# Kernel optimization log

Measured on AMD Instinct MI355X. Metric: run time of the kernel, lower is better.

Reference implementation:

```python
import jax, jax.numpy as jnp
import numpy as np
from jax.scipy.special import erf

# synthetic covalent radii table (original imports `covalent_radii`, e.g. from ase)
COV_RADII = jnp.asarray(0.3 + 0.02 * np.arange(100), dtype=jnp.float32)

B_MOL = 1024   # molecules per batch
N_ATOM = 128   # atoms per molecule (equal-sized ragged batch, atoms sorted by molecule)
N_ELEM = 10


def setup_inputs() -> dict:
    key = jax.random.key(0)
    ks = jax.random.split(key, 6)
    N = B_MOL * N_ATOM
    return {
        "eneg": jax.random.normal(ks[0], (N, 1), jnp.float32),
        "positions": jax.random.normal(ks[1], (N, 3), jnp.float32) * 3.0,
        "node_attrs": jax.random.uniform(ks[2], (N, N_ELEM), jnp.float32),
        "hardness": jax.random.uniform(ks[3], (N_ELEM,), jnp.float32),
        "total_charge": jax.random.normal(ks[4], (B_MOL,), jnp.float32),
        "batch": jnp.repeat(jnp.arange(B_MOL), N_ATOM),          # sorted molecule ids
        "atomic_numbers": jax.random.randint(ks[5], (N,), 1, 90),
    }


def reference(eneg, positions, node_attrs, hardness, total_charge, batch, atomic_numbers):
    # atoms are sorted by molecule with equal molecule sizes, so the ragged
    # python loop of the original collapses to a batched [B, n, ...] computation.
    B = total_charge.shape[0]
    N = positions.shape[0]
    n = N // B
    sqrt_pi = jnp.sqrt(jnp.asarray(np.pi, jnp.float32))
    sqrt_2 = jnp.sqrt(jnp.asarray(2.0, jnp.float32))

    pos = positions.reshape(B, n, 3)
    Z = atomic_numbers.reshape(B, n)
    atom_idx = jnp.argmax(node_attrs, axis=1).reshape(B, n)

    r = COV_RADII[Z]                                     # [B, n]
    diag_vals = hardness[atom_idx] + 1.0 / (sqrt_pi * r)  # [B, n]
    sigma = jnp.square(r)                                # [B, n]
    gamma = jnp.sqrt(sigma[:, :, None] + sigma[:, None, :])  # [B, n, n]

    diff = pos[:, :, None, :] - pos[:, None, :, :]       # [B, n, n, 3]
    sq = jnp.sum(diff * diff, axis=-1)                   # [B, n, n]
    eye = jnp.eye(n, dtype=bool)
    dist = jnp.sqrt(jnp.where(eye, 1.0, sq))             # safe diag (overwritten below)

    A = erf(dist / (sqrt_2 * gamma)) / dist              # [B, n, n]
    A = jnp.where(eye, diag_vals[:, :, None], A)         # scatter hardness diagonal

    # augment with charge-conservation row/column of ones (corner = 1)
    A = jnp.concatenate([A, jnp.ones((B, n, 1), A.dtype)], axis=2)
    A = jnp.concatenate([A, jnp.ones((B, 1, n + 1), A.dtype)], axis=1)

    b = jnp.concatenate([-eneg.reshape(B, n, 1),
                         total_charge.reshape(B, 1, 1)], axis=1)  # [B, n+1, 1]

    x = jnp.linalg.solve(A, b)                           # batched small solves
    return x[:, :n, 0].reshape(-1)                       # partial charges, [N]
```

## Files before the change

kernel.cpp:

```cpp
#include <hip/hip_runtime.h>
#include <math.h>

#define NMOL  1024
#define N     128
#define NELEM 10
#define BLOCK 256
#define PW    8
#define NPAN  16
#define PSTR  12
#define USTR  132

typedef __attribute__((ext_vector_type(4))) float f4;


__global__ __launch_bounds__(BLOCK, 2) void ceq_solve_kernel(
    const float* __restrict__ eneg,
    const float* __restrict__ positions,
    const float* __restrict__ node_attrs,
    const float* __restrict__ hardness,
    const float* __restrict__ total_charge,
    const int*   __restrict__ atomic_numbers,
    float* __restrict__ out)
{
    __shared__ __align__(16) float P[2][N * PSTR];
    __shared__ __align__(16) float Up[2][PW * USTR];
    __shared__ __align__(16) float Ublk[2][NPAN][PW][PW];
    __shared__ float Dinv[2][PW], Dd[2][PW];
    __shared__ float rhsY[2][N], rhsZ[2][N];
    __shared__ float sxY[2][N], sxZ[2][N];
    __shared__ float px[2][N], py[2][N], pz[2][N], sg[2][N], dgv[2][N];
    __shared__ float lamS[2];

    const int tid  = threadIdx.x;
    const int lane = tid & 63;
    const int g    = tid >> 7;
    const int gt   = tid & 127;
    const int wv   = (tid >> 6) & 1;
    const int r0   = 2 * lane;
    const int r1   = r0 + 1;
    const int mol  = 2 * blockIdx.x + g;
    const int base = mol * N;

    {
        const int i = gt;
        const int Z = atomic_numbers[base + i];
        const float rad = 0.3f + 0.02f * (float)Z;
        sg[g][i] = rad * rad;
        const float* na = node_attrs + (size_t)(base + i) * NELEM;
        float best = na[0]; int bi = 0;
        #pragma unroll
        for (int e = 1; e < NELEM; ++e) {
            float v = na[e];
            if (v > best) { best = v; bi = e; }
        }
        dgv[g][i] = hardness[bi] + 0.5641895835477563f / rad;
        const float* p = positions + (size_t)(base + i) * 3;
        px[g][i] = p[0]; py[g][i] = p[1]; pz[g][i] = p[2];
        rhsY[g][i] = -eneg[base + i];
        rhsZ[g][i] = 1.0f;
    }
    __syncthreads();

    f4 Ar0[16], Ar1[16];
    {
        const float x0 = px[g][r0], y0 = py[g][r0], z0 = pz[g][r0];
        const float s0 = sg[g][r0], d0 = dgv[g][r0];
        const float x1 = px[g][r1], y1 = py[g][r1], z1 = pz[g][r1];
        const float s1 = sg[g][r1], d1 = dgv[g][r1];
        #pragma unroll
        for (int c = 0; c < 16; ++c) {
            const int jb = 16 * (c >> 1) + 8 * wv + 4 * (c & 1);
            f4 v0, v1;
            #pragma unroll
            for (int e = 0; e < 4; ++e) {
                const int j = jb + e;
                float a0, a1;
                if (j == r0) a0 = d0;
                else {
                    const float dx = x0 - px[g][j], dy = y0 - py[g][j], dz = z0 - pz[g][j];
                    const float d = sqrtf(dx * dx + dy * dy + dz * dz);
                    a0 = erff(d / (1.4142135623730951f * sqrtf(s0 + sg[g][j]))) / d;
                }
                if (j == r1) a1 = d1;
                else {
                    const float dx = x1 - px[g][j], dy = y1 - py[g][j], dz = z1 - pz[g][j];
                    const float d = sqrtf(dx * dx + dy * dy + dz * dz);
                    a1 = erff(d / (1.4142135623730951f * sqrtf(s1 + sg[g][j]))) / d;
                }
                ((float*)&v0)[e] = a0;
                ((float*)&v1)[e] = a1;
            }
            Ar0[c] = v0;
            Ar1[c] = v1;
        }
    }

    for (int p = 0; p < NPAN; ++p) {
        const int k0 = PW * p;
        const int q  = (p >> 1) & 7;

        if (wv == (p & 1) && lane >= 4 * p) {
            f4 a00, a01, a10, a11;
            switch (q) {
                case 0:  a00 = Ar0[0];  a01 = Ar0[1];  a10 = Ar1[0];  a11 = Ar1[1];  break;
                case 1:  a00 = Ar0[2];  a01 = Ar0[3];  a10 = Ar1[2];  a11 = Ar1[3];  break;
                case 2:  a00 = Ar0[4];  a01 = Ar0[5];  a10 = Ar1[4];  a11 = Ar1[5];  break;
                case 3:  a00 = Ar0[6];  a01 = Ar0[7];  a10 = Ar1[6];  a11 = Ar1[7];  break;
                case 4:  a00 = Ar0[8];  a01 = Ar0[9];  a10 = Ar1[8];  a11 = Ar1[9];  break;
                case 5:  a00 = Ar0[10]; a01 = Ar0[11]; a10 = Ar1[10]; a11 = Ar1[11]; break;
                case 6:  a00 = Ar0[12]; a01 = Ar0[13]; a10 = Ar1[12]; a11 = Ar1[13]; break;
                default: a00 = Ar0[14]; a01 = Ar0[15]; a10 = Ar1[14]; a11 = Ar1[15]; break;
            }
            if (lane >= 4 * p + 4) {
                *(f4*)&P[g][r0 * PSTR + 0] = a00; *(f4*)&P[g][r0 * PSTR + 4] = a01;
                *(f4*)&P[g][r1 * PSTR + 0] = a10; *(f4*)&P[g][r1 * PSTR + 4] = a11;
            } else {
                float u0[PW] = { a00.x, a00.y, a00.z, a00.w, a01.x, a01.y, a01.z, a01.w };
                float u1[PW] = { a10.x, a10.y, a10.z, a10.w, a11.x, a11.y, a11.z, a11.w };
                float ry0 = rhsY[g][r0], rz0 = rhsZ[g][r0];
                float ry1 = rhsY[g][r1], rz1 = rhsZ[g][r1];
                const int rl = lane - 4 * p;
                #pragma unroll
                for (int kk = 0; kk < PW; ++kk) {
                    const int src = 4 * p + (kk >> 1);
                    float pr[PW];
                    #pragma unroll
                    for (int j = kk; j < PW; ++j)
                        pr[j] = __shfl((kk & 1) ? u1[j] : u0[j], src);
                    const float cY = __shfl((kk & 1) ? ry1 : ry0, src);
                    const float cZ = __shfl((kk & 1) ? rz1 : rz0, src);
                    const float dinv = 1.0f / pr[kk];
                    if (2 * rl > kk) {
                        const float m = u0[kk] * dinv; u0[kk] = m;
                        #pragma unroll
                        for (int j = kk + 1; j < PW; ++j) u0[j] -= m * pr[j];
                        ry0 -= m * cY; rz0 -= m * cZ;
                    }
                    if (2 * rl + 1 > kk) {
                        const float m = u1[kk] * dinv; u1[kk] = m;
                        #pragma unroll
                        for (int j = kk + 1; j < PW; ++j) u1[j] -= m * pr[j];
                        ry1 -= m * cY; rz1 -= m * cZ;
                    }
                    if (rl == (kk >> 1)) { Dinv[g][kk] = dinv; Dd[g][kk] = pr[kk]; }
                }
                f4 w0 = { u0[0], u0[1], u0[2], u0[3] }, w1 = { u0[4], u0[5], u0[6], u0[7] };
                *(f4*)&Ublk[g][p][2 * rl][0] = w0; *(f4*)&Ublk[g][p][2 * rl][4] = w1;
                f4 w2 = { u1[0], u1[1], u1[2], u1[3] }, w3 = { u1[4], u1[5], u1[6], u1[7] };
                *(f4*)&Ublk[g][p][2 * rl + 1][0] = w2; *(f4*)&Ublk[g][p][2 * rl + 1][4] = w3;
                rhsY[g][r0] = ry0; rhsZ[g][r0] = rz0;
                rhsY[g][r1] = ry1; rhsZ[g][r1] = rz1;
            }
        }
        __syncthreads();

        const int nb = (N - PW) - k0;
        if (gt < nb) {
            const int i = k0 + PW + gt;
            f4 a = *(const f4*)&P[g][i * PSTR], b = *(const f4*)&P[g][i * PSTR + 4];
            float av[PW] = { a.x, a.y, a.z, a.w, b.x, b.y, b.z, b.w };
            float m[PW];
            #pragma unroll
            for (int j = 0; j < PW; ++j) {
                float acc = av[j];
                #pragma unroll
                for (int t = 0; t < j; ++t) acc -= m[t] * Ublk[g][p][t][j];
                m[j] = acc * Dinv[g][j];
            }
            f4 ma = { m[0], m[1], m[2], m[3] }, mb = { m[4], m[5], m[6], m[7] };
            *(f4*)&P[g][i * PSTR]     = ma;
            *(f4*)&P[g][i * PSTR + 4] = mb;
            #pragma unroll
            for (int u = 0; u < PW; ++u) Up[g][u * USTR + i] = m[u] * Dd[g][u];
            float ry = rhsY[g][i], rz = rhsZ[g][i];
            #pragma unroll
            for (int t = 0; t < PW; ++t) {
                ry -= m[t] * rhsY[g][k0 + t];
                rz -= m[t] * rhsZ[g][k0 + t];
            }
            rhsY[g][i] = ry; rhsZ[g][i] = rz;
        }
        __syncthreads();

        if (lane >= 4 * p && lane < 4 * p + 4) {
            const int u0 = r0 - k0, u1 = u0 + 1;
            #pragma unroll
            for (int c = 0; c < 16; ++c) {
                const int t  = 2 * (c >> 1) + wv;
                const int gc = 4 * (c >> 1) + 2 * wv + (c & 1);
                if (t > p) {
                    Ar0[c] = *(const f4*)&Up[g][u0 * USTR + 4 * gc];
                    Ar1[c] = *(const f4*)&Up[g][u1 * USTR + 4 * gc];
                }
            }
        }
        const bool hasmat = (14 + wv) > p;
        if (hasmat && lane >= 4 * p + 4) {
            float lA0[PW], lA1[PW];
            {
                f4 a = *(const f4*)&P[g][r0 * PSTR], b = *(const f4*)&P[g][r0 * PSTR + 4];
                lA0[0]=a.x; lA0[1]=a.y; lA0[2]=a.z; lA0[3]=a.w;
                lA0[4]=b.x; lA0[5]=b.y; lA0[6]=b.z; lA0[7]=b.w;
                f4 c2 = *(const f4*)&P[g][r1 * PSTR], d2 = *(const f4*)&P[g][r1 * PSTR + 4];
                lA1[0]=c2.x; lA1[1]=c2.y; lA1[2]=c2.z; lA1[3]=c2.w;
                lA1[4]=d2.x; lA1[5]=d2.y; lA1[6]=d2.z; lA1[7]=d2.w;
            }
            #pragma unroll
            for (int c = 0; c < 16; ++c) {
                const int t  = 2 * (c >> 1) + wv;
                const int gc = 4 * (c >> 1) + 2 * wv + (c & 1);
                if (t > p) {
                    f4 acc0 = Ar0[c], acc1 = Ar1[c];
                    #pragma unroll
                    for (int u = 0; u < PW; ++u) {
                        const f4 uv = *(const f4*)&Up[g][u * USTR + 4 * gc];
                        acc0 -= uv * lA0[u];
                        acc1 -= uv * lA1[u];
                    }
                    Ar0[c] = acc0; Ar1[c] = acc1;
                }
            }
        }
        __syncthreads();
    }

    for (int pb = NPAN - 1; pb >= 0; --pb) {
        const int k0 = PW * pb;
        if (tid < 4) {
            const int gg = tid >> 1;
            float* rhs = (tid & 1) ? rhsZ[gg] : rhsY[gg];
            float* sx  = (tid & 1) ? sxZ[gg]  : sxY[gg];
            float x[PW];
            #pragma unroll
            for (int kk = PW - 1; kk >= 0; --kk) {
                float acc = rhs[k0 + kk];
                #pragma unroll
                for (int jj = kk + 1; jj < PW; ++jj) acc -= Ublk[gg][pb][kk][jj] * x[jj];
                x[kk] = acc / Ublk[gg][pb][kk][kk];
                sx[k0 + kk] = x[kk];
            }
        }
        __syncthreads();
        if (wv == (pb & 1) && lane < 4 * pb) {
            f4 a00, a01, a10, a11;
            switch ((pb >> 1) & 7) {
                case 0:  a00 = Ar0[0];  a01 = Ar0[1];  a10 = Ar1[0];  a11 = Ar1[1];  break;
                case 1:  a00 = Ar0[2];  a01 = Ar0[3];  a10 = Ar1[2];  a11 = Ar1[3];  break;
                case 2:  a00 = Ar0[4];  a01 = Ar0[5];  a10 = Ar1[4];  a11 = Ar1[5];  break;
                case 3:  a00 = Ar0[6];  a01 = Ar0[7];  a10 = Ar1[6];  a11 = Ar1[7];  break;
                case 4:  a00 = Ar0[8];  a01 = Ar0[9];  a10 = Ar1[8];  a11 = Ar1[9];  break;
                case 5:  a00 = Ar0[10]; a01 = Ar0[11]; a10 = Ar1[10]; a11 = Ar1[11]; break;
                case 6:  a00 = Ar0[12]; a01 = Ar0[13]; a10 = Ar1[12]; a11 = Ar1[13]; break;
                default: a00 = Ar0[14]; a01 = Ar0[15]; a10 = Ar1[14]; a11 = Ar1[15]; break;
            }
            float yy0 = rhsY[g][r0], yy1 = rhsY[g][r1];
            float zz0 = rhsZ[g][r0], zz1 = rhsZ[g][r1];
            yy0 -= a00.x*sxY[g][k0]   + a00.y*sxY[g][k0+1] + a00.z*sxY[g][k0+2] + a00.w*sxY[g][k0+3]
                 + a01.x*sxY[g][k0+4] + a01.y*sxY[g][k0+5] + a01.z*sxY[g][k0+6] + a01.w*sxY[g][k0+7];
            yy1 -= a10.x*sxY[g][k0]   + a10.y*sxY[g][k0+1] + a10.z*sxY[g][k0+2] + a10.w*sxY[g][k0+3]
                 + a11.x*sxY[g][k0+4] + a11.y*sxY[g][k0+5] + a11.z*sxY[g][k0+6] + a11.w*sxY[g][k0+7];
            zz0 -= a00.x*sxZ[g][k0]   + a00.y*sxZ[g][k0+1] + a00.z*sxZ[g][k0+2] + a00.w*sxZ[g][k0+3]
                 + a01.x*sxZ[g][k0+4] + a01.y*sxZ[g][k0+5] + a01.z*sxZ[g][k0+6] + a01.w*sxZ[g][k0+7];
            zz1 -= a10.x*sxZ[g][k0]   + a10.y*sxZ[g][k0+1] + a10.z*sxZ[g][k0+2] + a10.w*sxZ[g][k0+3]
                 + a11.x*sxZ[g][k0+4] + a11.y*sxZ[g][k0+5] + a11.z*sxZ[g][k0+6] + a11.w*sxZ[g][k0+7];
            rhsY[g][r0] = yy0; rhsY[g][r1] = yy1;
            rhsZ[g][r0] = zz0; rhsZ[g][r1] = zz1;
        }
        __syncthreads();
    }

    if (wv == 0) {
        float vY = sxY[g][lane] + sxY[g][lane + 64];
        float vZ = sxZ[g][lane] + sxZ[g][lane + 64];
        #pragma unroll
        for (int off = 32; off; off >>= 1) {
            vY += __shfl_xor(vY, off);
            vZ += __shfl_xor(vZ, off);
        }
        if (lane == 0) lamS[g] = (vY - total_charge[mol]) / (vZ - 1.0f);
    }
    __syncthreads();
    out[base + gt] = sxY[g][gt] - lamS[g] * sxZ[g][gt];
}

extern "C" void kernel_launch(void* const* d_in, const int* in_sizes, int n_in,
                              void* d_out, int out_size, void* d_ws, size_t ws_size,
                              hipStream_t stream) {
    const float* eneg           = (const float*)d_in[0];
    const float* positions      = (const float*)d_in[1];
    const float* node_attrs     = (const float*)d_in[2];
    const float* hardness       = (const float*)d_in[3];
    const float* total_charge   = (const float*)d_in[4];
    const int*   atomic_numbers = (const int*)d_in[6];
    float* out = (float*)d_out;

    ceq_solve_kernel<<<NMOL / 2, BLOCK, 0, stream>>>(
        eneg, positions, node_attrs, hardness, total_charge, atomic_numbers, out);
}
```

Measured before the change: 214.5 us.

## Widen LU panel width to 16 and alias staging arrays into panel buffer

Doubles the blocked LU panel width from 8 to 16, halving the number of panels and the barrier-separated factor/update phases. The register-resident matrix tile is remapped to a new column layout, and the back-substitution dot products are vectorised. Per-atom staging arrays now alias the panel shared buffer to offset the larger panel and Ublk storage, which needs an extra barrier. In exchange the serial in-panel factorization and triangular solves get longer, and register pressure rises.

Result: slower. 253.5 us (+18.2%).

```diff
diff --git a/kernel.cpp b/kernel.cpp
--- a/kernel.cpp
+++ b/kernel.cpp
@@ -5,9 +5,9 @@
 #define N     128
 #define NELEM 10
 #define BLOCK 256
-#define PW    8
-#define NPAN  16
-#define PSTR  12
+#define PW    16
+#define NPAN  8
+#define PSTR  20
 #define USTR  132
 
 typedef __attribute__((ext_vector_type(4))) float f4;
@@ -26,9 +26,8 @@
     __shared__ __align__(16) float Up[2][PW * USTR];
     __shared__ __align__(16) float Ublk[2][NPAN][PW][PW];
     __shared__ float Dinv[2][PW], Dd[2][PW];
-    __shared__ float rhsY[2][N], rhsZ[2][N];
-    __shared__ float sxY[2][N], sxZ[2][N];
-    __shared__ float px[2][N], py[2][N], pz[2][N], sg[2][N], dgv[2][N];
+    __shared__ __align__(16) float rhsY[2][N], rhsZ[2][N];
+    __shared__ __align__(16) float sxY[2][N], sxZ[2][N];
     __shared__ float lamS[2];
 
     const int tid  = threadIdx.x;
@@ -41,11 +40,17 @@
     const int mol  = 2 * blockIdx.x + g;
     const int base = mol * N;
 
+    float* px  = &P[g][0 * N];
+    float* py  = &P[g][1 * N];
+    float* pz  = &P[g][2 * N];
+    float* sg  = &P[g][3 * N];
+    float* dgv = &P[g][4 * N];
+
     {
         const int i = gt;
         const int Z = atomic_numbers[base + i];
         const float rad = 0.3f + 0.02f * (float)Z;
-        sg[g][i] = rad * rad;
+        sg[i] = rad * rad;
         const float* na = node_attrs + (size_t)(base + i) * NELEM;
         float best = na[0]; int bi = 0;
         #pragma unroll
@@ -53,9 +58,9 @@
             float v = na[e];
             if (v > best) { best = v; bi = e; }
         }
-        dgv[g][i] = hardness[bi] + 0.5641895835477563f / rad;
+        dgv[i] = hardness[bi] + 0.5641895835477563f / rad;
         const float* p = positions + (size_t)(base + i) * 3;
-        px[g][i] = p[0]; py[g][i] = p[1]; pz[g][i] = p[2];
+        px[i] = p[0]; py[i] = p[1]; pz[i] = p[2];
         rhsY[g][i] = -eneg[base + i];
         rhsZ[g][i] = 1.0f;
     }
@@ -63,13 +68,13 @@
 
     f4 Ar0[16], Ar1[16];
     {
-        const float x0 = px[g][r0], y0 = py[g][r0], z0 = pz[g][r0];
-        const float s0 = sg[g][r0], d0 = dgv[g][r0];
-        const float x1 = px[g][r1], y1 = py[g][r1], z1 = pz[g][r1];
-        const float s1 = sg[g][r1], d1 = dgv[g][r1];
+        const float x0 = px[r0], y0 = py[r0], z0 = pz[r0];
+        const float s0 = sg[r0], d0 = dgv[r0];
+        const float x1 = px[r1], y1 = py[r1], z1 = pz[r1];
+        const float s1 = sg[r1], d1 = dgv[r1];
         #pragma unroll
         for (int c = 0; c < 16; ++c) {
-            const int jb = 16 * (c >> 1) + 8 * wv + 4 * (c & 1);
+            const int jb = 32 * (c >> 2) + 16 * wv + 4 * (c & 3);
             f4 v0, v1;
             #pragma unroll
             for (int e = 0; e < 4; ++e) {
@@ -77,15 +82,15 @@
                 float a0, a1;
                 if (j == r0) a0 = d0;
                 else {
-                    const float dx = x0 - px[g][j], dy = y0 - py[g][j], dz = z0 - pz[g][j];
+                    const float dx = x0 - px[j], dy = y0 - py[j], dz = z0 - pz[j];
                     const float d = sqrtf(dx * dx + dy * dy + dz * dz);
-                    a0 = erff(d / (1.4142135623730951f * sqrtf(s0 + sg[g][j]))) / d;
+                    a0 = erff(d / (1.4142135623730951f * sqrtf(s0 + sg[j]))) / d;
                 }
                 if (j == r1) a1 = d1;
                 else {
-                    const float dx = x1 - px[g][j], dy = y1 - py[g][j], dz = z1 - pz[g][j];
+                    const float dx = x1 - px[j], dy = y1 - py[j], dz = z1 - pz[j];
                     const float d = sqrtf(dx * dx + dy * dy + dz * dz);
-                    a1 = erff(d / (1.4142135623730951f * sqrtf(s1 + sg[g][j]))) / d;
+                    a1 = erff(d / (1.4142135623730951f * sqrtf(s1 + sg[j]))) / d;
                 }
                 ((float*)&v0)[e] = a0;
                 ((float*)&v1)[e] = a1;
@@ -94,35 +99,40 @@
             Ar1[c] = v1;
         }
     }
+    __syncthreads();
 
     for (int p = 0; p < NPAN; ++p) {
         const int k0 = PW * p;
-        const int q  = (p >> 1) & 7;
-
-        if (wv == (p & 1) && lane >= 4 * p) {
-            f4 a00, a01, a10, a11;
-            switch (q) {
-                case 0:  a00 = Ar0[0];  a01 = Ar0[1];  a10 = Ar1[0];  a11 = Ar1[1];  break;
-                case 1:  a00 = Ar0[2];  a01 = Ar0[3];  a10 = Ar1[2];  a11 = Ar1[3];  break;
-                case 2:  a00 = Ar0[4];  a01 = Ar0[5];  a10 = Ar1[4];  a11 = Ar1[5];  break;
-                case 3:  a00 = Ar0[6];  a01 = Ar0[7];  a10 = Ar1[6];  a11 = Ar1[7];  break;
-                case 4:  a00 = Ar0[8];  a01 = Ar0[9];  a10 = Ar1[8];  a11 = Ar1[9];  break;
-                case 5:  a00 = Ar0[10]; a01 = Ar0[11]; a10 = Ar1[10]; a11 = Ar1[11]; break;
-                case 6:  a00 = Ar0[12]; a01 = Ar0[13]; a10 = Ar1[12]; a11 = Ar1[13]; break;
-                default: a00 = Ar0[14]; a01 = Ar0[15]; a10 = Ar1[14]; a11 = Ar1[15]; break;
-            }
-            if (lane >= 4 * p + 4) {
-                *(f4*)&P[g][r0 * PSTR + 0] = a00; *(f4*)&P[g][r0 * PSTR + 4] = a01;
-                *(f4*)&P[g][r1 * PSTR + 0] = a10; *(f4*)&P[g][r1 * PSTR + 4] = a11;
+        const int k  = p >> 1;
+
+        if (wv == (p & 1) && lane >= 8 * p) {
+            f4 a0, a1, a2, a3, b0, b1, b2, b3;
+            switch (k) {
+                case 0:  a0=Ar0[0];  a1=Ar0[1];  a2=Ar0[2];  a3=Ar0[3];
+                         b0=Ar1[0];  b1=Ar1[1];  b2=Ar1[2];  b3=Ar1[3];  break;
+                case 1:  a0=Ar0[4];  a1=Ar0[5];  a2=Ar0[6];  a3=Ar0[7];
+                         b0=Ar1[4];  b1=Ar1[5];  b2=Ar1[6];  b3=Ar1[7];  break;
+                case 2:  a0=Ar0[8];  a1=Ar0[9];  a2=Ar0[10]; a3=Ar0[11];
+                         b0=Ar1[8];  b1=Ar1[9];  b2=Ar1[10]; b3=Ar1[11]; break;
+                default: a0=Ar0[12]; a1=Ar0[13]; a2=Ar0[14]; a3=Ar0[15];
+                         b0=Ar1[12]; b1=Ar1[13]; b2=Ar1[14]; b3=Ar1[15]; break;
+            }
+            if (lane >= 8 * p + 8) {
+                *(f4*)&P[g][r0 * PSTR + 0] = a0; *(f4*)&P[g][r0 * PSTR + 4]  = a1;
+                *(f4*)&P[g][r0 * PSTR + 8] = a2; *(f4*)&P[g][r0 * PSTR + 12] = a3;
+                *(f4*)&P[g][r1 * PSTR + 0] = b0; *(f4*)&P[g][r1 * PSTR + 4]  = b1;
+                *(f4*)&P[g][r1 * PSTR + 8] = b2; *(f4*)&P[g][r1 * PSTR + 12] = b3;
             } else {
-                float u0[PW] = { a00.x, a00.y, a00.z, a00.w, a01.x, a01.y, a01.z, a01.w };
-                float u1[PW] = { a10.x, a10.y, a10.z, a10.w, a11.x, a11.y, a11.z, a11.w };
+                float u0[PW] = { a0.x,a0.y,a0.z,a0.w, a1.x,a1.y,a1.z,a1.w,
+                                 a2.x,a2.y,a2.z,a2.w, a3.x,a3.y,a3.z,a3.w };
+                float u1[PW] = { b0.x,b0.y,b0.z,b0.w, b1.x,b1.y,b1.z,b1.w,
+                                 b2.x,b2.y,b2.z,b2.w, b3.x,b3.y,b3.z,b3.w };
                 float ry0 = rhsY[g][r0], rz0 = rhsZ[g][r0];
                 float ry1 = rhsY[g][r1], rz1 = rhsZ[g][r1];
-                const int rl = lane - 4 * p;
+                const int rl = lane - 8 * p;
                 #pragma unroll
                 for (int kk = 0; kk < PW; ++kk) {
-                    const int src = 4 * p + (kk >> 1);
+                    const int src = 8 * p + (kk >> 1);
                     float pr[PW];
                     #pragma unroll
                     for (int j = kk; j < PW; ++j)
@@ -144,10 +154,15 @@
                     }
                     if (rl == (kk >> 1)) { Dinv[g][kk] = dinv; Dd[g][kk] = pr[kk]; }
                 }
-                f4 w0 = { u0[0], u0[1], u0[2], u0[3] }, w1 = { u0[4], u0[5], u0[6], u0[7] };
-                *(f4*)&Ublk[g][p][2 * rl][0] = w0; *(f4*)&Ublk[g][p][2 * rl][4] = w1;
-                f4 w2 = { u1[0], u1[1], u1[2], u1[3] }, w3 = { u1[4], u1[5], u1[6], u1[7] };
-                *(f4*)&Ublk[g][p][2 * rl + 1][0] = w2; *(f4*)&Ublk[g][p][2 * rl + 1][4] = w3;
+                f4 w;
+                w = (f4){u0[0],u0[1],u0[2],u0[3]};    *(f4*)&Ublk[g][p][2*rl][0]  = w;
+                w = (f4){u0[4],u0[5],u0[6],u0[7]};    *(f4*)&Ublk[g][p][2*rl][4]  = w;
+                w = (f4){u0[8],u0[9],u0[10],u0[11]};  *(f4*)&Ublk[g][p][2*rl][8]  = w;
+                w = (f4){u0[12],u0[13],u0[14],u0[15]};*(f4*)&Ublk[g][p][2*rl][12] = w;
+                w = (f4){u1[0],u1[1],u1[2],u1[3]};    *(f4*)&Ublk[g][p][2*rl+1][0]  = w;
+                w = (f4){u1[4],u1[5],u1[6],u1[7]};    *(f4*)&Ublk[g][p][2*rl+1][4]  = w;
+                w = (f4){u1[8],u1[9],u1[10],u1[11]};  *(f4*)&Ublk[g][p][2*rl+1][8]  = w;
+                w = (f4){u1[12],u1[13],u1[14],u1[15]};*(f4*)&Ublk[g][p][2*rl+1][12] = w;
                 rhsY[g][r0] = ry0; rhsZ[g][r0] = rz0;
                 rhsY[g][r1] = ry1; rhsZ[g][r1] = rz1;
             }
@@ -157,8 +172,10 @@
         const int nb = (N - PW) - k0;
         if (gt < nb) {
             const int i = k0 + PW + gt;
-            f4 a = *(const f4*)&P[g][i * PSTR], b = *(const f4*)&P[g][i * PSTR + 4];
-            float av[PW] = { a.x, a.y, a.z, a.w, b.x, b.y, b.z, b.w };
+            f4 A0 = *(const f4*)&P[g][i * PSTR + 0], A1 = *(const f4*)&P[g][i * PSTR + 4];
+            f4 A2 = *(const f4*)&P[g][i * PSTR + 8], A3 = *(const f4*)&P[g][i * PSTR + 12];
+            float av[PW] = { A0.x,A0.y,A0.z,A0.w, A1.x,A1.y,A1.z,A1.w,
+                             A2.x,A2.y,A2.z,A2.w, A3.x,A3.y,A3.z,A3.w };
             float m[PW];
             #pragma unroll
             for (int j = 0; j < PW; ++j) {
@@ -167,9 +184,11 @@
                 for (int t = 0; t < j; ++t) acc -= m[t] * Ublk[g][p][t][j];
                 m[j] = acc * Dinv[g][j];
             }
-            f4 ma = { m[0], m[1], m[2], m[3] }, mb = { m[4], m[5], m[6], m[7] };
-            *(f4*)&P[g][i * PSTR]     = ma;
-            *(f4*)&P[g][i * PSTR + 4] = mb;
+            f4 w;
+            w = (f4){m[0],m[1],m[2],m[3]};     *(f4*)&P[g][i * PSTR + 0]  = w;
+            w = (f4){m[4],m[5],m[6],m[7]};     *(f4*)&P[g][i * PSTR + 4]  = w;
+            w = (f4){m[8],m[9],m[10],m[11]};   *(f4*)&P[g][i * PSTR + 8]  = w;
+            w = (f4){m[12],m[13],m[14],m[15]}; *(f4*)&P[g][i * PSTR + 12] = w;
             #pragma unroll
             for (int u = 0; u < PW; ++u) Up[g][u * USTR + i] = m[u] * Dd[g][u];
             float ry = rhsY[g][i], rz = rhsZ[g][i];
@@ -182,38 +201,44 @@
         }
         __syncthreads();
 
-        if (lane >= 4 * p && lane < 4 * p + 4) {
-            const int u0 = r0 - k0, u1 = u0 + 1;
+        if (lane >= 8 * p && lane < 8 * p + 8) {
+            const int u0r = r0 - k0, u1r = u0r + 1;
             #pragma unroll
             for (int c = 0; c < 16; ++c) {
-                const int t  = 2 * (c >> 1) + wv;
-                const int gc = 4 * (c >> 1) + 2 * wv + (c & 1);
+                const int t  = 2 * (c >> 2) + wv;
+                const int jb = 32 * (c >> 2) + 16 * wv + 4 * (c & 3);
                 if (t > p) {
-                    Ar0[c] = *(const f4*)&Up[g][u0 * USTR + 4 * gc];
-                    Ar1[c] = *(const f4*)&Up[g][u1 * USTR + 4 * gc];
-                }
-            }
-        }
-        const bool hasmat = (14 + wv) > p;
-        if (hasmat && lane >= 4 * p + 4) {
+                    Ar0[c] = *(const f4*)&Up[g][u0r * USTR + jb];
+                    Ar1[c] = *(const f4*)&Up[g][u1r * USTR + jb];
+                }
+            }
+        }
+        const bool hasmat = (6 + wv) > p;
+        if (hasmat && lane >= 8 * p + 8) {
             float lA0[PW], lA1[PW];
             {
-                f4 a = *(const f4*)&P[g][r0 * PSTR], b = *(const f4*)&P[g][r0 * PSTR + 4];
+                f4 a = *(const f4*)&P[g][r0 * PSTR + 0], b = *(const f4*)&P[g][r0 * PSTR + 4];
+                f4 c2 = *(const f4*)&P[g][r0 * PSTR + 8], d2 = *(const f4*)&P[g][r0 * PSTR + 12];
                 lA0[0]=a.x; lA0[1]=a.y; lA0[2]=a.z; lA0[3]=a.w;
                 lA0[4]=b.x; lA0[5]=b.y; lA0[6]=b.z; lA0[7]=b.w;
-                f4 c2 = *(const f4*)&P[g][r1 * PSTR], d2 = *(const f4*)&P[g][r1 * PSTR + 4];
-                lA1[0]=c2.x; lA1[1]=c2.y; lA1[2]=c2.z; lA1[3]=c2.w;
-                lA1[4]=d2.x; lA1[5]=d2.y; lA1[6]=d2.z; lA1[7]=d2.w;
+                lA0[8]=c2.x; lA0[9]=c2.y; lA0[10]=c2.z; lA0[11]=c2.w;
+                lA0[12]=d2.x; lA0[13]=d2.y; lA0[14]=d2.z; lA0[15]=d2.w;
+                f4 e = *(const f4*)&P[g][r1 * PSTR + 0], f = *(const f4*)&P[g][r1 * PSTR + 4];
+                f4 h = *(const f4*)&P[g][r1 * PSTR + 8], i2 = *(const f4*)&P[g][r1 * PSTR + 12];
+                lA1[0]=e.x; lA1[1]=e.y; lA1[2]=e.z; lA1[3]=e.w;
+                lA1[4]=f.x; lA1[5]=f.y; lA1[6]=f.z; lA1[7]=f.w;
+                lA1[8]=h.x; lA1[9]=h.y; lA1[10]=h.z; lA1[11]=h.w;
+                lA1[12]=i2.x; lA1[13]=i2.y; lA1[14]=i2.z; lA1[15]=i2.w;
             }
             #pragma unroll
             for (int c = 0; c < 16; ++c) {
-                const int t  = 2 * (c >> 1) + wv;
-                const int gc = 4 * (c >> 1) + 2 * wv + (c & 1);
+                const int t  = 2 * (c >> 2) + wv;
+                const int jb = 32 * (c >> 2) + 16 * wv + 4 * (c & 3);
                 if (t > p) {
                     f4 acc0 = Ar0[c], acc1 = Ar1[c];
                     #pragma unroll
                     for (int u = 0; u < PW; ++u) {
-                        const f4 uv = *(const f4*)&Up[g][u * USTR + 4 * gc];
+                        const f4 uv = *(const f4*)&Up[g][u * USTR + jb];
                         acc0 -= uv * lA0[u];
                         acc1 -= uv * lA1[u];
                     }
@@ -241,30 +266,30 @@
             }
         }
         __syncthreads();
-        if (wv == (pb & 1) && lane < 4 * pb) {
-            f4 a00, a01, a10, a11;
-            switch ((pb >> 1) & 7) {
-                case 0:  a00 = Ar0[0];  a01 = Ar0[1];  a10 = Ar1[0];  a11 = Ar1[1];  break;
-                case 1:  a00 = Ar0[2];  a01 = Ar0[3];  a10 = Ar1[2];  a11 = Ar1[3];  break;
-                case 2:  a00 = Ar0[4];  a01 = Ar0[5];  a10 = Ar1[4];  a11 = Ar1[5];  break;
-                case 3:  a00 = Ar0[6];  a01 = Ar0[7];  a10 = Ar1[6];  a11 = Ar1[7];  break;
-                case 4:  a00 = Ar0[8];  a01 = Ar0[9];  a10 = Ar1[8];  a11 = Ar1[9];  break;
-                case 5:  a00 = Ar0[10]; a01 = Ar0[11]; a10 = Ar1[10]; a11 = Ar1[11]; break;
-                case 6:  a00 = Ar0[12]; a01 = Ar0[13]; a10 = Ar1[12]; a11 = Ar1[13]; break;
-                default: a00 = Ar0[14]; a01 = Ar0[15]; a10 = Ar1[14]; a11 = Ar1[15]; break;
-            }
-            float yy0 = rhsY[g][r0], yy1 = rhsY[g][r1];
-            float zz0 = rhsZ[g][r0], zz1 = rhsZ[g][r1];
-            yy0 -= a00.x*sxY[g][k0]   + a00.y*sxY[g][k0+1] + a00.z*sxY[g][k0+2] + a00.w*sxY[g][k0+3]
-                 + a01.x*sxY[g][k0+4] + a01.y*sxY[g][k0+5] + a01.z*sxY[g][k0+6] + a01.w*sxY[g][k0+7];
-            yy1 -= a10.x*sxY[g][k0]   + a10.y*sxY[g][k0+1] + a10.z*sxY[g][k0+2] + a10.w*sxY[g][k0+3]
-                 + a11.x*sxY[g][k0+4] + a11.y*sxY[g][k0+5] + a11.z*sxY[g][k0+6] + a11.w*sxY[g][k0+7];
-            zz0 -= a00.x*sxZ[g][k0]   + a00.y*sxZ[g][k0+1] + a00.z*sxZ[g][k0+2] + a00.w*sxZ[g][k0+3]
-                 + a01.x*sxZ[g][k0+4] + a01.y*sxZ[g][k0+5] + a01.z*sxZ[g][k0+6] + a01.w*sxZ[g][k0+7];
-            zz1 -= a10.x*sxZ[g][k0]   + a10.y*sxZ[g][k0+1] + a10.z*sxZ[g][k0+2] + a10.w*sxZ[g][k0+3]
-                 + a11.x*sxZ[g][k0+4] + a11.y*sxZ[g][k0+5] + a11.z*sxZ[g][k0+6] + a11.w*sxZ[g][k0+7];
-            rhsY[g][r0] = yy0; rhsY[g][r1] = yy1;
-            rhsZ[g][r0] = zz0; rhsZ[g][r1] = zz1;
+        if (wv == (pb & 1) && lane < 8 * pb) {
+            f4 a0, a1, a2, a3, b0, b1, b2, b3;
+            switch (pb >> 1) {
+                case 0:  a0=Ar0[0];  a1=Ar0[1];  a2=Ar0[2];  a3=Ar0[3];
+                         b0=Ar1[0];  b1=Ar1[1];  b2=Ar1[2];  b3=Ar1[3];  break;
+                case 1:  a0=Ar0[4];  a1=Ar0[5];  a2=Ar0[6];  a3=Ar0[7];
+                         b0=Ar1[4];  b1=Ar1[5];  b2=Ar1[6];  b3=Ar1[7];  break;
+                case 2:  a0=Ar0[8];  a1=Ar0[9];  a2=Ar0[10]; a3=Ar0[11];
+                         b0=Ar1[8];  b1=Ar1[9];  b2=Ar1[10]; b3=Ar1[11]; break;
+                default: a0=Ar0[12]; a1=Ar0[13]; a2=Ar0[14]; a3=Ar0[15];
+                         b0=Ar1[12]; b1=Ar1[13]; b2=Ar1[14]; b3=Ar1[15]; break;
+            }
+            const f4 sy0 = *(const f4*)&sxY[g][k0 + 0],  sy1 = *(const f4*)&sxY[g][k0 + 4];
+            const f4 sy2 = *(const f4*)&sxY[g][k0 + 8],  sy3 = *(const f4*)&sxY[g][k0 + 12];
+            const f4 sz0 = *(const f4*)&sxZ[g][k0 + 0],  sz1 = *(const f4*)&sxZ[g][k0 + 4];
+            const f4 sz2 = *(const f4*)&sxZ[g][k0 + 8],  sz3 = *(const f4*)&sxZ[g][k0 + 12];
+            f4 ty0 = a0 * sy0 + a1 * sy1 + a2 * sy2 + a3 * sy3;
+            f4 ty1 = b0 * sy0 + b1 * sy1 + b2 * sy2 + b3 * sy3;
+            f4 tz0 = a0 * sz0 + a1 * sz1 + a2 * sz2 + a3 * sz3;
+            f4 tz1 = b0 * sz0 + b1 * sz1 + b2 * sz2 + b3 * sz3;
+            rhsY[g][r0] -= ty0.x + ty0.y + ty0.z + ty0.w;
+            rhsY[g][r1] -= ty1.x + ty1.y + ty1.z + ty1.w;
+            rhsZ[g][r0] -= tz0.x + tz0.y + tz0.z + tz0.w;
+            rhsZ[g][r1] -= tz1.x + tz1.y + tz1.z + tz1.w;
         }
         __syncthreads();
     }
```
